# Performance work log

Measured on AMD Instinct MI355X. Metric: run time of the kernel, lower is better.

## Reference

```python
import jax, jax.numpy as jnp
import numpy as np

D_MODEL = 1024
N_HEADS = 16
HEAD_DIM = D_MODEL // N_HEADS
SCALE = HEAD_DIM ** -0.5
MIN_VAL = jnp.finfo(jnp.float32).min


def setup_inputs() -> dict:
    key = jax.random.key(0)
    ks = jax.random.split(key, 7)
    B, T = 1, 2048
    s = D_MODEL ** -0.5
    return {
        "x": jax.random.normal(ks[0], (B, T, D_MODEL), dtype=jnp.float32),
        "Wq": jax.random.normal(ks[1], (D_MODEL, D_MODEL), dtype=jnp.float32) * s,
        "Wk1": jax.random.normal(ks[2], (D_MODEL, D_MODEL), dtype=jnp.float32) * s,
        "Wk2": jax.random.normal(ks[3], (D_MODEL, D_MODEL), dtype=jnp.float32) * s,
        "Wv": jax.random.normal(ks[4], (D_MODEL, D_MODEL), dtype=jnp.float32) * s,
        "Wo": jax.random.normal(ks[5], (D_MODEL, D_MODEL), dtype=jnp.float32) * s,
        "lambda_logit": jnp.zeros((N_HEADS,), dtype=jnp.float32),  # logit(0.5)=0
    }


def _split_heads(y):
    B, T, _ = y.shape
    return y.reshape(B, T, N_HEADS, HEAD_DIM).transpose(0, 2, 1, 3)  # [B,H,T,hd]


def reference(x, Wq, Wk1, Wk2, Wv, Wo, lambda_logit):
    B, T, _ = x.shape
    q = _split_heads(x @ Wq.T)
    k1 = _split_heads(x @ Wk1.T)
    k2 = _split_heads(x @ Wk2.T)
    v = _split_heads(x @ Wv.T)

    s1 = jnp.einsum("bhqd,bhkd->bhqk", q, k1) * SCALE
    s2 = jnp.einsum("bhqd,bhkd->bhqk", q, k2) * SCALE

    causal = jnp.arange(T)[None, :] <= jnp.arange(T)[:, None]  # [T,T] keep mask
    s1 = jnp.where(causal[None, None], s1, MIN_VAL)
    s2 = jnp.where(causal[None, None], s2, MIN_VAL)

    attn_exp = jax.nn.softmax(s1, axis=-1)
    attn_noise = jax.nn.softmax(s2, axis=-1)
    lam = jax.nn.sigmoid(lambda_logit)[None, :, None, None]
    attn = attn_exp - lam * attn_noise
    denom = jnp.maximum(jnp.sum(jnp.abs(attn), axis=-1, keepdims=True), 1e-6)
    attn = attn / denom

    out = jnp.einsum("bhqk,bhkd->bhqd", attn, v)
    out = out.transpose(0, 2, 1, 3).reshape(B, T, D_MODEL)
    return out @ Wo.T
```

## Files before the change

### kernel.cpp

```cpp
#include <hip/hip_runtime.h>

#define T_SEQ 2048
#define DM 1024
#define NH 16
#define HD 64
#define SC2 0.1803368801111731f
#define LS 72

typedef unsigned short u16;
typedef unsigned int u32;
typedef __attribute__((ext_vector_type(8))) short bf16x8;
typedef __attribute__((ext_vector_type(4))) float f32x4;

static __device__ __forceinline__ f32x4 mfma16(bf16x8 a, bf16x8 b, f32x4 c) {
    return __builtin_amdgcn_mfma_f32_16x16x32_bf16(a, b, c, 0, 0, 0);
}
static __device__ __forceinline__ float bf2f(u16 u) {
    union { u32 i; float f; } v; v.i = ((u32)u) << 16; return v.f;
}
static __device__ __forceinline__ u16 f2bf(float f) {
    union { float f; u32 i; } v; v.f = f;
    u32 x = v.i;
    x += 0x7FFFu + ((x >> 16) & 1u);
    return (u16)(x >> 16);
}
static __device__ __forceinline__ u16 f2bf_t(float f) {
    union { float f; u32 i; } v; v.f = f;
    return (u16)(v.i >> 16);
}
static __device__ __forceinline__ u32 pk2(float lo, float hi) {
    return (u32)f2bf(lo) | ((u32)f2bf(hi) << 16);
}
static __device__ __forceinline__ uint4 ld8(const void* src, size_t idx, int f) {
    if (f) return *(const uint4*)((const u16*)src + idx);
    const float* s = (const float*)src + idx;
    uint4 a = *(const uint4*)s;
    uint4 b = *(const uint4*)(s + 4);
    const float* af = (const float*)&a;
    const float* bf = (const float*)&b;
    uint4 r;
    r.x = pk2(af[0], af[1]); r.y = pk2(af[2], af[3]);
    r.z = pk2(bf[0], bf[1]); r.w = pk2(bf[2], bf[3]);
    return r;
}
static __device__ __forceinline__ float qsum16(float v) {
#pragma unroll
    for (int o = 1; o < 16; o <<= 1) v += __shfl_xor(v, o, 64);
    return v;
}
static __device__ __forceinline__ float ex2(float x) {
    return __builtin_amdgcn_exp2f(x);
}

static __device__ __forceinline__ void gl16(const u16* g, u16* l) {
    __builtin_amdgcn_global_load_lds(
        (const __attribute__((address_space(1))) void*)g,
        (__attribute__((address_space(3))) void*)l,
        16, 0, 0);
}

template <int NISS>
static __device__ __forceinline__ void stage_async(const u16* src, size_t row0,
                                                   size_t lds_, size_t col0,
                                                   u16* dst, int tid) {
#pragma unroll
    for (int it = 0; it < NISS; it++) {
        int r = it * 32 + (tid >> 3);
        int cg = (tid & 7) ^ (r & 7);
        gl16(&src[(row0 + r) * lds_ + col0 + cg * 8], &dst[(it * 256 + tid) * 8]);
    }
}
template <int NISS>
static __device__ __forceinline__ void stage_sync(const void* src, size_t row0,
                                                  size_t lds_, size_t col0,
                                                  u16* dst, int tid, int f) {
#pragma unroll
    for (int it = 0; it < NISS; it++) {
        int r = it * 32 + (tid >> 3);
        int cg = (tid & 7) ^ (r & 7);
        *(uint4*)(&dst[(it * 256 + tid) * 8]) =
            ld8(src, (row0 + r) * lds_ + col0 + cg * 8, f);
    }
}
static __device__ __forceinline__ bf16x8 frag(const u16* buf, int R, int co) {
    return *(const bf16x8*)(&buf[R * 64 + co]);
}

static __device__ __forceinline__ int detect_flag(const u16* x, int tid,
                                                  int* tot ) {
    if (tid == 0) *tot = 0;
    __syncthreads();
    int c = 0;
#pragma unroll
    for (int i = 0; i < 4; i++) {
        u16 v = x[2 * (tid * 4 + i)];
        int e = (v >> 7) & 0xFF;
        c += (e >= 110 && e <= 140) ? 1 : 0;
    }
    atomicAdd(tot, c);
    __syncthreads();
    return (*tot >= 512) ? 1 : 0;
}

__global__ __launch_bounds__(256) void qkv_gemm(
    const void* __restrict__ xs, const void* __restrict__ wq,
    const void* __restrict__ wk1, const void* __restrict__ wk2,
    const void* __restrict__ wv, int* __restrict__ flag,
    u16* __restrict__ qd, u16* __restrict__ k1d, u16* __restrict__ k2d,
    u16* __restrict__ vtd) {
    __shared__ __align__(16) u16 As[2][128 * 64];
    __shared__ __align__(16) u16 Bs[2][128 * 64];
    __shared__ int flg_tot;

    const int tid = threadIdx.x;
    const int f = detect_flag((const u16*)xs, tid, &flg_tot);
    if (blockIdx.x == 0 && blockIdx.y == 0 && tid == 0) *flag = f;

    const int w = blockIdx.x >> 3;
    const int n0 = (blockIdx.x & 7) * 128;
    const int m0 = blockIdx.y * 128;
    const void* Bpv = (w == 0) ? wq : (w == 1) ? wk1 : (w == 2) ? wk2 : wv;
    const u16* xb = (const u16*)xs;
    const u16* Bb = (const u16*)Bpv;

    const int lane = tid & 63, wave = tid >> 6;
    const int lr = lane & 15, quad = lane >> 4;
    const int wm = (wave >> 1) * 64, wn = (wave & 1) * 64;
    const int sw = lr & 7;

    f32x4 acc[4][4];
#pragma unroll
    for (int i = 0; i < 4; i++)
#pragma unroll
        for (int j = 0; j < 4; j++) acc[i][j] = (f32x4){0.f, 0.f, 0.f, 0.f};

    if (f) {
        stage_async<4>(xb, m0, DM, 0, As[0], tid);
        stage_async<4>(Bb, n0, DM, 0, Bs[0], tid);
    }
    for (int k0 = 0; k0 < DM; k0 += 64) {
        const int cur = (k0 >> 6) & 1;
        __syncthreads();
        if (f) {
            if (k0 + 64 < DM) {
                stage_async<4>(xb, m0, DM, k0 + 64, As[cur ^ 1], tid);
                stage_async<4>(Bb, n0, DM, k0 + 64, Bs[cur ^ 1], tid);
            }
        } else {
            stage_sync<4>(xs, m0, DM, k0, As[cur], tid, 0);
            stage_sync<4>(Bpv, n0, DM, k0, Bs[cur], tid, 0);
            __syncthreads();
        }
#pragma unroll
        for (int kk = 0; kk < 2; kk++) {
            const int co = ((kk * 4 + quad) ^ sw) * 8;
            bf16x8 af[4], bfr[4];
#pragma unroll
            for (int i = 0; i < 4; i++) af[i] = frag(As[cur], wm + i * 16 + lr, co);
#pragma unroll
            for (int j = 0; j < 4; j++) bfr[j] = frag(Bs[cur], wn + j * 16 + lr, co);
#pragma unroll
            for (int i = 0; i < 4; i++)
#pragma unroll
                for (int j = 0; j < 4; j++) acc[i][j] = mfma16(af[i], bfr[j], acc[i][j]);
        }
    }

#pragma unroll
    for (int i = 0; i < 4; i++)
#pragma unroll
        for (int j = 0; j < 4; j++)
#pragma unroll
            for (int r = 0; r < 4; r++) {
                int t = m0 + wm + i * 16 + quad * 4 + r;
                int o = n0 + wn + j * 16 + lr;
                float val = acc[i][j][r];
                if (w == 0) val *= SC2;
                u16 vbits = f2bf(val);
                int hh = o >> 6, d0 = o & 63;
                if (w == 3)
                    vtd[((size_t)hh * HD + d0) * T_SEQ + t] = vbits;
                else
                    ((w == 0) ? qd : (w == 1) ? k1d : k2d)[((size_t)hh * T_SEQ + t) * HD + d0] = vbits;
            }
}

#define ATTN_MAP()                                            \
    const int b = blockIdx.x;                                 \
    const int par = b >> 9;                                   \
    const int rem = b & 511;                                  \
    const int h = rem & 15;                                   \
    const int bi = rem >> 4;                                  \
    const int qt = (bi < 16) ? bi : 47 - bi;                  \
    const int t0 = qt * 64;                                   \
    const int tid = threadIdx.x;                              \
    const int lane = tid & 63, wave = tid >> 6;               \
    const int lr = lane & 15, quad = lane >> 4;               \
    const int wm = wave * 16;                                 \
    const int sw = lr & 7;

__global__ __launch_bounds__(256) void attn_a(
    const u16* __restrict__ qg, const u16* __restrict__ k1g,
    const u16* __restrict__ k2g, float* __restrict__ zp) {
    __shared__ __align__(16) u16 k1s[64 * 64];
    __shared__ __align__(16) u16 k2s[64 * 64];
    ATTN_MAP();

    const u16* qh = qg + (size_t)h * T_SEQ * HD;
    const u16* k1h = k1g + (size_t)h * T_SEQ * HD;
    const u16* k2h = k2g + (size_t)h * T_SEQ * HD;

    bf16x8 aq[2];
#pragma unroll
    for (int kk = 0; kk < 2; kk++)
        aq[kk] = *(const bf16x8*)(&qh[(size_t)(t0 + wm + lr) * HD + kk * 32 + quad * 8]);

    float z1a[4] = {0.f, 0.f, 0.f, 0.f}, z2a[4] = {0.f, 0.f, 0.f, 0.f};

    for (int kt = par; kt <= qt; kt += 4) {
        __syncthreads();
        stage_async<2>(k1h, (size_t)kt * 64, HD, 0, k1s, tid);
        stage_async<2>(k2h, (size_t)kt * 64, HD, 0, k2s, tid);
        __syncthreads();

        f32x4 sa[4], sb[4];
#pragma unroll
        for (int j = 0; j < 4; j++) { sa[j] = (f32x4){0.f,0.f,0.f,0.f}; sb[j] = (f32x4){0.f,0.f,0.f,0.f}; }
#pragma unroll
        for (int kk = 0; kk < 2; kk++) {
            const int co = ((kk * 4 + quad) ^ sw) * 8;
#pragma unroll
            for (int j = 0; j < 4; j++) {
                sa[j] = mfma16(aq[kk], frag(k1s, j * 16 + lr, co), sa[j]);
                sb[j] = mfma16(aq[kk], frag(k2s, j * 16 + lr, co), sb[j]);
            }
        }

        if (kt < qt) {
#pragma unroll
            for (int r = 0; r < 4; r++)
#pragma unroll
                for (int j = 0; j < 4; j++) {
                    z1a[r] += ex2(sa[j][r]);
                    z2a[r] += ex2(sb[j][r]);
                }
        } else {
#pragma unroll
            for (int r = 0; r < 4; r++) {
                const int grow = t0 + wm + quad * 4 + r;
#pragma unroll
                for (int j = 0; j < 4; j++) {
                    int gcol = kt * 64 + j * 16 + lr;
                    if (gcol <= grow) {
                        z1a[r] += ex2(sa[j][r]);
                        z2a[r] += ex2(sb[j][r]);
                    }
                }
            }
        }
    }

#pragma unroll
    for (int r = 0; r < 4; r++) {
        float s1 = qsum16(z1a[r]);
        float s2 = qsum16(z2a[r]);
        if (lr == 0) {
            int row = t0 + wm + quad * 4 + r;
            zp[((size_t)(par * 2 + 0) * NH + h) * T_SEQ + row] = s1;
            zp[((size_t)(par * 2 + 1) * NH + h) * T_SEQ + row] = s2;
        }
    }
}

__global__ __launch_bounds__(256) void attn_b(
    const u16* __restrict__ qg, const u16* __restrict__ k1g,
    const u16* __restrict__ k2g, const u16* __restrict__ vtg,
    const float* __restrict__ zp, const void* __restrict__ lamsrc,
    const int* __restrict__ flag,
    float* __restrict__ dpart, u16* __restrict__ opart) {
    __shared__ __align__(16) u16 k1s[64 * 64];
    __shared__ __align__(16) u16 k2s[64 * 64];
    __shared__ __align__(16) u16 vs[64 * 64];
    __shared__ __align__(16) u16 ps[4][16 * LS];
    ATTN_MAP();

    const int f = *flag;
    float lamlogit = f ? bf2f(((const u16*)lamsrc)[h]) : ((const float*)lamsrc)[h];
    const float lam = 1.0f / (1.0f + __expf(-lamlogit));

    const u16* qh = qg + (size_t)h * T_SEQ * HD;
    const u16* k1h = k1g + (size_t)h * T_SEQ * HD;
    const u16* k2h = k2g + (size_t)h * T_SEQ * HD;
    const u16* vh = vtg + (size_t)h * HD * T_SEQ;

    bf16x8 aq[2];
#pragma unroll
    for (int kk = 0; kk < 2; kk++)
        aq[kk] = *(const bf16x8*)(&qh[(size_t)(t0 + wm + lr) * HD + kk * 32 + quad * 8]);

    float z1l[4], z2l[4];
#pragma unroll
    for (int r = 0; r < 4; r++) {
        int row = t0 + wm + quad * 4 + r;
        float z1 = 0.f, z2 = 0.f;
#pragma unroll
        for (int p = 0; p < 4; p++) {
            z1 += zp[((size_t)(p * 2 + 0) * NH + h) * T_SEQ + row];
            z2 += zp[((size_t)(p * 2 + 1) * NH + h) * T_SEQ + row];
        }
        z1l[r] = -__log2f(z1);
        z2l[r] = __log2f(lam) - __log2f(z2);
    }

    f32x4 oac[4];
#pragma unroll
    for (int j = 0; j < 4; j++) oac[j] = (f32x4){0.f, 0.f, 0.f, 0.f};
    float dacc[4] = {0.f, 0.f, 0.f, 0.f};

    for (int kt = par; kt <= qt; kt += 2) {
        __syncthreads();
        stage_async<2>(k1h, (size_t)kt * 64, HD, 0, k1s, tid);
        stage_async<2>(k2h, (size_t)kt * 64, HD, 0, k2s, tid);
        stage_async<2>(vh, 0, T_SEQ, (size_t)kt * 64, vs, tid);
        __syncthreads();

        f32x4 sa[4], sb[4];
#pragma unroll
        for (int j = 0; j < 4; j++) { sa[j] = (f32x4){0.f,0.f,0.f,0.f}; sb[j] = (f32x4){0.f,0.f,0.f,0.f}; }
#pragma unroll
        for (int kk = 0; kk < 2; kk++) {
            const int co = ((kk * 4 + quad) ^ sw) * 8;
#pragma unroll
            for (int j = 0; j < 4; j++) {
                sa[j] = mfma16(aq[kk], frag(k1s, j * 16 + lr, co), sa[j]);
                sb[j] = mfma16(aq[kk], frag(k2s, j * 16 + lr, co), sb[j]);
            }
        }

        if (kt < qt) {
#pragma unroll
            for (int r = 0; r < 4; r++)
#pragma unroll
                for (int j = 0; j < 4; j++) {
                    float p = ex2(sa[j][r] + z1l[r]) - ex2(sb[j][r] + z2l[r]);
                    dacc[r] += fabsf(p);
                    ps[wave][(quad * 4 + r) * LS + j * 16 + lr] = f2bf_t(p);
                }
        } else {
#pragma unroll
            for (int r = 0; r < 4; r++) {
                const int grow = t0 + wm + quad * 4 + r;
#pragma unroll
                for (int j = 0; j < 4; j++) {
                    int gcol = kt * 64 + j * 16 + lr;
                    float p = 0.f;
                    if (gcol <= grow)
                        p = ex2(sa[j][r] + z1l[r]) - ex2(sb[j][r] + z2l[r]);
                    dacc[r] += fabsf(p);
                    ps[wave][(quad * 4 + r) * LS + j * 16 + lr] = f2bf_t(p);
                }
            }
        }

#pragma unroll
        for (int kk = 0; kk < 2; kk++) {
            bf16x8 pa = *(const bf16x8*)(&ps[wave][lr * LS + kk * 32 + quad * 8]);
            const int co = ((kk * 4 + quad) ^ sw) * 8;
#pragma unroll
            for (int j = 0; j < 4; j++)
                oac[j] = mfma16(pa, frag(vs, j * 16 + lr, co), oac[j]);
        }
    }

#pragma unroll
    for (int r = 0; r < 4; r++) {
        float ds = qsum16(dacc[r]);
        if (lr == 0) {
            int row = t0 + wm + quad * 4 + r;
            dpart[((size_t)par * NH + h) * T_SEQ + row] = ds;
        }
    }
#pragma unroll
    for (int j = 0; j < 4; j++)
#pragma unroll
        for (int r = 0; r < 4; r++) {
            int row = t0 + wm + quad * 4 + r;
            opart[(size_t)par * T_SEQ * DM + (size_t)row * DM + h * HD + j * 16 + lr] =
                f2bf(oac[j][r]);
        }
}

__global__ __launch_bounds__(256) void normalize_o(
    const u16* __restrict__ opart, const float* __restrict__ dpart,
    u16* __restrict__ ao) {
    int g = blockIdx.x * 256 + threadIdx.x;
    int t = g >> 7;
    int cc = g & 127;
    int d0 = cc * 8;
    int h = d0 >> 6;
    float dsum = dpart[(size_t)h * T_SEQ + t] + dpart[(size_t)(NH + h) * T_SEQ + t];
    float rs = 1.f / fmaxf(dsum, 1e-6f);
    uint4 a = *(const uint4*)(&opart[(size_t)t * DM + d0]);
    uint4 bqq = *(const uint4*)(&opart[(size_t)T_SEQ * DM + (size_t)t * DM + d0]);
    const u32* au = (const u32*)&a;
    const u32* bu = (const u32*)&bqq;
    uint4 out;
    u32* ou = (u32*)&out;
#pragma unroll
    for (int i = 0; i < 4; i++) {
        float lo = (bf2f((u16)(au[i] & 0xFFFF)) + bf2f((u16)(bu[i] & 0xFFFF))) * rs;
        float hi = (bf2f((u16)(au[i] >> 16)) + bf2f((u16)(bu[i] >> 16))) * rs;
        ou[i] = pk2(lo, hi);
    }
    *(uint4*)(&ao[(size_t)t * DM + d0]) = out;
}

__global__ __launch_bounds__(256) void out_gemm(
    const u16* __restrict__ ab, const void* __restrict__ wo,
    const int* __restrict__ flag, void* __restrict__ outp) {
    __shared__ __align__(16) u16 As[2][64 * 64];
    __shared__ __align__(16) u16 Bs[2][64 * 64];

    const int f = *flag;
    const int n0 = blockIdx.x * 64;
    const int m0 = blockIdx.y * 64;
    const u16* wb = (const u16*)wo;
    const int tid = threadIdx.x;
    const int lane = tid & 63, wave = tid >> 6;
    const int lr = lane & 15, quad = lane >> 4;
    const int wm = (wave >> 1) * 32, wn = (wave & 1) * 32;
    const int sw = lr & 7;

    f32x4 acc[2][2];
#pragma unroll
    for (int i = 0; i < 2; i++)
#pragma unroll
        for (int j = 0; j < 2; j++) acc[i][j] = (f32x4){0.f, 0.f, 0.f, 0.f};

    if (f) {
        stage_async<2>(ab, m0, DM, 0, As[0], tid);
        stage_async<2>(wb, n0, DM, 0, Bs[0], tid);
    }
    for (int k0 = 0; k0 < DM; k0 += 64) {
        const int cur = (k0 >> 6) & 1;
        __syncthreads();
        if (f) {
            if (k0 + 64 < DM) {
                stage_async<2>(ab, m0, DM, k0 + 64, As[cur ^ 1], tid);
                stage_async<2>(wb, n0, DM, k0 + 64, Bs[cur ^ 1], tid);
            }
        } else {
            stage_sync<2>(ab, m0, DM, k0, As[cur], tid, 1);
            stage_sync<2>(wo, n0, DM, k0, Bs[cur], tid, 0);
            __syncthreads();
        }
#pragma unroll
        for (int kk = 0; kk < 2; kk++) {
            const int co = ((kk * 4 + quad) ^ sw) * 8;
            bf16x8 af[2], bfr[2];
#pragma unroll
            for (int i = 0; i < 2; i++) af[i] = frag(As[cur], wm + i * 16 + lr, co);
#pragma unroll
            for (int j = 0; j < 2; j++) bfr[j] = frag(Bs[cur], wn + j * 16 + lr, co);
#pragma unroll
            for (int i = 0; i < 2; i++)
#pragma unroll
                for (int j = 0; j < 2; j++) acc[i][j] = mfma16(af[i], bfr[j], acc[i][j]);
        }
    }

#pragma unroll
    for (int i = 0; i < 2; i++)
#pragma unroll
        for (int j = 0; j < 2; j++)
#pragma unroll
            for (int r = 0; r < 4; r++) {
                int t = m0 + wm + i * 16 + quad * 4 + r;
                int o = n0 + wn + j * 16 + lr;
                float val = acc[i][j][r];
                if (f)
                    ((u16*)outp)[(size_t)t * DM + o] = f2bf(val);
                else
                    ((float*)outp)[(size_t)t * DM + o] = val;
            }
}

extern "C" void kernel_launch(void* const* d_in, const int* in_sizes, int n_in,
                              void* d_out, int out_size, void* d_ws, size_t ws_size,
                              hipStream_t stream) {
    char* ws = (char*)d_ws;
    int* flag = (int*)(ws + 0);
    float* zp    = (float*)(ws + ((size_t)1 << 20));
    float* dpart = (float*)(ws + ((size_t)2 << 20));
    u16* qd  = (u16*)(ws + ((size_t)16 << 20));
    u16* k1d = (u16*)(ws + ((size_t)20 << 20));
    u16* k2d = (u16*)(ws + ((size_t)24 << 20));
    u16* vtd = (u16*)(ws + ((size_t)28 << 20));
    u16* ao  = (u16*)(ws + ((size_t)32 << 20));
    u16* opart = (u16*)(ws + ((size_t)36 << 20));

    qkv_gemm<<<dim3(32, 16), 256, 0, stream>>>(d_in[0], d_in[1], d_in[2], d_in[3],
                                               d_in[4], flag, qd, k1d, k2d, vtd);
    attn_a<<<dim3(2048), 256, 0, stream>>>(qd, k1d, k2d, zp);
    attn_b<<<dim3(1024), 256, 0, stream>>>(qd, k1d, k2d, vtd, zp, d_in[6], flag,
                                           dpart, opart);
    normalize_o<<<dim3(1024), 256, 0, stream>>>(opart, dpart, ao);
    out_gemm<<<dim3(16, 32), 256, 0, stream>>>(ao, d_in[5], flag, d_out);
}
```

Baseline: 200.4 us.

## Pre-convert fp32 inputs to bf16 so GEMMs always use async LDS staging

```diff
diff --git a/kernel.cpp b/kernel.cpp
--- a/kernel.cpp
+++ b/kernel.cpp
@@ -31,18 +31,6 @@
 static __device__ __forceinline__ u32 pk2(float lo, float hi) {
     return (u32)f2bf(lo) | ((u32)f2bf(hi) << 16);
 }
-static __device__ __forceinline__ uint4 ld8(const void* src, size_t idx, int f) {
-    if (f) return *(const uint4*)((const u16*)src + idx);
-    const float* s = (const float*)src + idx;
-    uint4 a = *(const uint4*)s;
-    uint4 b = *(const uint4*)(s + 4);
-    const float* af = (const float*)&a;
-    const float* bf = (const float*)&b;
-    uint4 r;
-    r.x = pk2(af[0], af[1]); r.y = pk2(af[2], af[3]);
-    r.z = pk2(bf[0], bf[1]); r.w = pk2(bf[2], bf[3]);
-    return r;
-}
 static __device__ __forceinline__ float qsum16(float v) {
 #pragma unroll
     for (int o = 1; o < 16; o <<= 1) v += __shfl_xor(v, o, 64);
@@ -70,25 +58,15 @@
         gl16(&src[(row0 + r) * lds_ + col0 + cg * 8], &dst[(it * 256 + tid) * 8]);
     }
 }
-template <int NISS>
-static __device__ __forceinline__ void stage_sync(const void* src, size_t row0,
-                                                  size_t lds_, size_t col0,
-                                                  u16* dst, int tid, int f) {
-#pragma unroll
-    for (int it = 0; it < NISS; it++) {
-        int r = it * 32 + (tid >> 3);
-        int cg = (tid & 7) ^ (r & 7);
-        *(uint4*)(&dst[(it * 256 + tid) * 8]) =
-            ld8(src, (row0 + r) * lds_ + col0 + cg * 8, f);
-    }
-}
 static __device__ __forceinline__ bf16x8 frag(const u16* buf, int R, int co) {
     return *(const bf16x8*)(&buf[R * 64 + co]);
 }
 
-static __device__ __forceinline__ int detect_flag(const u16* x, int tid,
-                                                  int* tot ) {
-    if (tid == 0) *tot = 0;
+__global__ __launch_bounds__(256) void detect_dtype(const u16* __restrict__ x,
+                                                    int* __restrict__ flag) {
+    __shared__ int tot;
+    const int tid = threadIdx.x;
+    if (tid == 0) tot = 0;
     __syncthreads();
     int c = 0;
 #pragma unroll
@@ -97,31 +75,66 @@
         int e = (v >> 7) & 0xFF;
         c += (e >= 110 && e <= 140) ? 1 : 0;
     }
-    atomicAdd(tot, c);
+    atomicAdd(&tot, c);
     __syncthreads();
-    return (*tot >= 512) ? 1 : 0;
+    if (tid == 0) *flag = (tot >= 512) ? 1 : 0;
+}
+
+__global__ __launch_bounds__(256) void cvt_bf16(
+    const int* __restrict__ flag,
+    const float* __restrict__ x, const float* __restrict__ wq,
+    const float* __restrict__ wk1, const float* __restrict__ wk2,
+    const float* __restrict__ wv, const float* __restrict__ wo,
+    u16* __restrict__ xc, u16* __restrict__ wqc, u16* __restrict__ wk1c,
+    u16* __restrict__ wk2c, u16* __restrict__ wvc, u16* __restrict__ woc) {
+    if (*flag) return;
+    const int b = blockIdx.x;
+    const int tid = threadIdx.x;
+    const float* src;
+    u16* dst;
+    int rel;
+    if (b < 1024)      { src = x;   dst = xc;   rel = b; }
+    else if (b < 1536) { src = wq;  dst = wqc;  rel = b - 1024; }
+    else if (b < 2048) { src = wk1; dst = wk1c; rel = b - 1536; }
+    else if (b < 2560) { src = wk2; dst = wk2c; rel = b - 2048; }
+    else if (b < 3072) { src = wv;  dst = wvc;  rel = b - 2560; }
+    else               { src = wo;  dst = woc;  rel = b - 3072; }
+    size_t idx = (size_t)rel * 2048 + (size_t)tid * 8;
+    const float* s = src + idx;
+    uint4 a = *(const uint4*)s;
+    uint4 bq = *(const uint4*)(s + 4);
+    const float* af = (const float*)&a;
+    const float* bf = (const float*)&bq;
+    uint4 r;
+    r.x = pk2(af[0], af[1]); r.y = pk2(af[2], af[3]);
+    r.z = pk2(bf[0], bf[1]); r.w = pk2(bf[2], bf[3]);
+    *(uint4*)(dst + idx) = r;
 }
 
 __global__ __launch_bounds__(256) void qkv_gemm(
-    const void* __restrict__ xs, const void* __restrict__ wq,
-    const void* __restrict__ wk1, const void* __restrict__ wk2,
-    const void* __restrict__ wv, int* __restrict__ flag,
+    const int* __restrict__ flag,
+    const void* __restrict__ x0, const void* __restrict__ wq0,
+    const void* __restrict__ wk10, const void* __restrict__ wk20,
+    const void* __restrict__ wv0,
+    const u16* __restrict__ xc, const u16* __restrict__ wqc,
+    const u16* __restrict__ wk1c, const u16* __restrict__ wk2c,
+    const u16* __restrict__ wvc,
     u16* __restrict__ qd, u16* __restrict__ k1d, u16* __restrict__ k2d,
     u16* __restrict__ vtd) {
     __shared__ __align__(16) u16 As[2][128 * 64];
     __shared__ __align__(16) u16 Bs[2][128 * 64];
-    __shared__ int flg_tot;
-
+
+    const int f = *flag;
     const int tid = threadIdx.x;
-    const int f = detect_flag((const u16*)xs, tid, &flg_tot);
-    if (blockIdx.x == 0 && blockIdx.y == 0 && tid == 0) *flag = f;
-
     const int w = blockIdx.x >> 3;
     const int n0 = (blockIdx.x & 7) * 128;
     const int m0 = blockIdx.y * 128;
-    const void* Bpv = (w == 0) ? wq : (w == 1) ? wk1 : (w == 2) ? wk2 : wv;
-    const u16* xb = (const u16*)xs;
-    const u16* Bb = (const u16*)Bpv;
+    const u16* xb = f ? (const u16*)x0 : xc;
+    const u16* Bb;
+    if (w == 0)      Bb = f ? (const u16*)wq0  : wqc;
+    else if (w == 1) Bb = f ? (const u16*)wk10 : wk1c;
+    else if (w == 2) Bb = f ? (const u16*)wk20 : wk2c;
+    else             Bb = f ? (const u16*)wv0  : wvc;
 
     const int lane = tid & 63, wave = tid >> 6;
     const int lr = lane & 15, quad = lane >> 4;
@@ -134,22 +147,14 @@
 #pragma unroll
         for (int j = 0; j < 4; j++) acc[i][j] = (f32x4){0.f, 0.f, 0.f, 0.f};
 
-    if (f) {
-        stage_async<4>(xb, m0, DM, 0, As[0], tid);
-        stage_async<4>(Bb, n0, DM, 0, Bs[0], tid);
-    }
+    stage_async<4>(xb, m0, DM, 0, As[0], tid);
+    stage_async<4>(Bb, n0, DM, 0, Bs[0], tid);
     for (int k0 = 0; k0 < DM; k0 += 64) {
         const int cur = (k0 >> 6) & 1;
         __syncthreads();
-        if (f) {
-            if (k0 + 64 < DM) {
-                stage_async<4>(xb, m0, DM, k0 + 64, As[cur ^ 1], tid);
-                stage_async<4>(Bb, n0, DM, k0 + 64, Bs[cur ^ 1], tid);
-            }
-        } else {
-            stage_sync<4>(xs, m0, DM, k0, As[cur], tid, 0);
-            stage_sync<4>(Bpv, n0, DM, k0, Bs[cur], tid, 0);
-            __syncthreads();
+        if (k0 + 64 < DM) {
+            stage_async<4>(xb, m0, DM, k0 + 64, As[cur ^ 1], tid);
+            stage_async<4>(Bb, n0, DM, k0 + 64, Bs[cur ^ 1], tid);
         }
 #pragma unroll
         for (int kk = 0; kk < 2; kk++) {
@@ -416,15 +421,16 @@
 }
 
 __global__ __launch_bounds__(256) void out_gemm(
-    const u16* __restrict__ ab, const void* __restrict__ wo,
-    const int* __restrict__ flag, void* __restrict__ outp) {
+    const u16* __restrict__ ab, const void* __restrict__ wo0,
+    const u16* __restrict__ woc, const int* __restrict__ flag,
+    void* __restrict__ outp) {
     __shared__ __align__(16) u16 As[2][64 * 64];
     __shared__ __align__(16) u16 Bs[2][64 * 64];
 
     const int f = *flag;
+    const u16* wb = f ? (const u16*)wo0 : woc;
     const int n0 = blockIdx.x * 64;
     const int m0 = blockIdx.y * 64;
-    const u16* wb = (const u16*)wo;
     const int tid = threadIdx.x;
     const int lane = tid & 63, wave = tid >> 6;
     const int lr = lane & 15, quad = lane >> 4;
@@ -437,22 +443,14 @@
 #pragma unroll
         for (int j = 0; j < 2; j++) acc[i][j] = (f32x4){0.f, 0.f, 0.f, 0.f};
 
-    if (f) {
-        stage_async<2>(ab, m0, DM, 0, As[0], tid);
-        stage_async<2>(wb, n0, DM, 0, Bs[0], tid);
-    }
+    stage_async<2>(ab, m0, DM, 0, As[0], tid);
+    stage_async<2>(wb, n0, DM, 0, Bs[0], tid);
     for (int k0 = 0; k0 < DM; k0 += 64) {
         const int cur = (k0 >> 6) & 1;
         __syncthreads();
-        if (f) {
-            if (k0 + 64 < DM) {
-                stage_async<2>(ab, m0, DM, k0 + 64, As[cur ^ 1], tid);
-                stage_async<2>(wb, n0, DM, k0 + 64, Bs[cur ^ 1], tid);
-            }
-        } else {
-            stage_sync<2>(ab, m0, DM, k0, As[cur], tid, 1);
-            stage_sync<2>(wo, n0, DM, k0, Bs[cur], tid, 0);
-            __syncthreads();
+        if (k0 + 64 < DM) {
+            stage_async<2>(ab, m0, DM, k0 + 64, As[cur ^ 1], tid);
+            stage_async<2>(wb, n0, DM, k0 + 64, Bs[cur ^ 1], tid);
         }
 #pragma unroll
         for (int kk = 0; kk < 2; kk++) {
@@ -498,12 +496,24 @@
     u16* vtd = (u16*)(ws + ((size_t)28 << 20));
     u16* ao  = (u16*)(ws + ((size_t)32 << 20));
     u16* opart = (u16*)(ws + ((size_t)36 << 20));
-
-    qkv_gemm<<<dim3(32, 16), 256, 0, stream>>>(d_in[0], d_in[1], d_in[2], d_in[3],
-                                               d_in[4], flag, qd, k1d, k2d, vtd);
+    u16* xc   = (u16*)(ws + ((size_t)44 << 20));
+    u16* wqc  = (u16*)(ws + ((size_t)48 << 20));
+    u16* wk1c = (u16*)(ws + ((size_t)50 << 20));
+    u16* wk2c = (u16*)(ws + ((size_t)52 << 20));
+    u16* wvc  = (u16*)(ws + ((size_t)54 << 20));
+    u16* woc  = (u16*)(ws + ((size_t)56 << 20));
+
+    detect_dtype<<<dim3(1), 256, 0, stream>>>((const u16*)d_in[0], flag);
+    cvt_bf16<<<dim3(3584), 256, 0, stream>>>(
+        flag, (const float*)d_in[0], (const float*)d_in[1], (const float*)d_in[2],
+        (const float*)d_in[3], (const float*)d_in[4], (const float*)d_in[5],
+        xc, wqc, wk1c, wk2c, wvc, woc);
+    qkv_gemm<<<dim3(32, 16), 256, 0, stream>>>(
+        flag, d_in[0], d_in[1], d_in[2], d_in[3], d_in[4],
+        xc, wqc, wk1c, wk2c, wvc, qd, k1d, k2d, vtd);
     attn_a<<<dim3(2048), 256, 0, stream>>>(qd, k1d, k2d, zp);
     attn_b<<<dim3(1024), 256, 0, stream>>>(qd, k1d, k2d, vtd, zp, d_in[6], flag,
                                            dpart, opart);
     normalize_o<<<dim3(1024), 256, 0, stream>>>(opart, dpart, ao);
-    out_gemm<<<dim3(16, 32), 256, 0, stream>>>(ao, d_in[5], flag, d_out);
-}
+    out_gemm<<<dim3(16, 32), 256, 0, stream>>>(ao, d_in[5], woc, flag, d_out);
+}
```

Result: faster. 192.5 us (-4.0%).
